# Performance work log

Hardware: AMD Instinct MI355X
Metric: run time of the kernel (lower is better)

The kernel has to match this reference:

```python
import jax, jax.numpy as jnp
import numpy as np

IN_DIM = 128; OUT_DIM = 128; H = 8; DK = OUT_DIM // H
N_A = 100000; N_B = 100000; E0 = 400000; E1 = 400000
NUM_TYPES = 2; NUM_REL = 2
EPS = 1e-9; LN_EPS = 1e-5


def setup_inputs() -> dict:
    key = jax.random.key(0)
    ks = jax.random.split(key, 16)
    s = 0.02
    xav = float(np.sqrt(6.0 / (DK + DK)))  # xavier_uniform bound for (dk, dk)
    inp = {}
    inp['x_a'] = jax.random.normal(ks[0], (N_A, IN_DIM), jnp.float32)
    inp['x_b'] = jax.random.normal(ks[1], (N_B, IN_DIM), jnp.float32)
    inp['ew0'] = jax.random.uniform(ks[2], (E0,), jnp.float32)
    inp['ew1'] = jax.random.uniform(ks[3], (E1,), jnp.float32)
    inp['src0'] = jax.random.randint(ks[4], (E0,), 0, N_A)
    inp['dst0'] = jax.random.randint(ks[5], (E0,), 0, N_B)
    inp['src1'] = jax.random.randint(ks[6], (E1,), 0, N_B)
    inp['dst1'] = jax.random.randint(ks[7], (E1,), 0, N_A)
    # per-node-type stacked linear params: [type, in, out]
    inp['Wk'] = jax.random.normal(ks[8], (NUM_TYPES, IN_DIM, OUT_DIM), jnp.float32) * s
    inp['bk'] = jnp.zeros((NUM_TYPES, OUT_DIM), jnp.float32)
    inp['Wq'] = jax.random.normal(ks[9], (NUM_TYPES, IN_DIM, OUT_DIM), jnp.float32) * s
    inp['bq'] = jnp.zeros((NUM_TYPES, OUT_DIM), jnp.float32)
    inp['Wv'] = jax.random.normal(ks[10], (NUM_TYPES, IN_DIM, OUT_DIM), jnp.float32) * s
    inp['bv'] = jnp.zeros((NUM_TYPES, OUT_DIM), jnp.float32)
    inp['Wa'] = jax.random.normal(ks[11], (NUM_TYPES, OUT_DIM, OUT_DIM), jnp.float32) * s
    inp['ba'] = jnp.zeros((NUM_TYPES, OUT_DIM), jnp.float32)
    inp['ln_g'] = jnp.ones((NUM_TYPES, OUT_DIM), jnp.float32)
    inp['ln_b'] = jnp.zeros((NUM_TYPES, OUT_DIM), jnp.float32)
    inp['rel_pri'] = jnp.ones((NUM_REL, H), jnp.float32)
    inp['rel_att'] = jax.random.uniform(ks[12], (NUM_REL, H, DK, DK), jnp.float32, -xav, xav)
    inp['rel_msg'] = jax.random.uniform(ks[13], (NUM_REL, H, DK, DK), jnp.float32, -xav, xav)
    inp['skip'] = jnp.ones((NUM_TYPES,), jnp.float32)
    return inp


def _edge_softmax(logits, dst, n_dst):
    # segment softmax over incoming edges of each dst node; logits: (E, H)
    m = jax.ops.segment_max(logits, dst, num_segments=n_dst)
    e = jnp.exp(logits - m[dst])
    s = jax.ops.segment_sum(e, dst, num_segments=n_dst)
    return e / s[dst]


def _relation(x_s, x_d, src, dst, ew, Wk_s, bk_s, Wq_d, bq_d, Wv_s, bv_s,
              ratt, rmsg, rpri, n_dst):
    # per-relation HGT attention -> aggregated dst messages (n_dst, H, DK)
    k = (x_s @ Wk_s + bk_s).reshape(-1, H, DK)
    k = jnp.einsum('nhd,hde->nhe', k, ratt)
    v = (x_s @ Wv_s + bv_s).reshape(-1, H, DK)
    v = jnp.einsum('nhd,hde->nhe', v, rmsg)
    q = (x_d @ Wq_d + bq_d).reshape(-1, H, DK)
    t = jnp.einsum('ehd,ehd->eh', q[dst], k[src])  # edge dot score (E, H)
    # dst-normalized edge weight -> additive log bias
    ew = jnp.clip(ew, 0.0)
    den = jax.ops.segment_sum(ew, dst, num_segments=n_dst)
    ewn = ew / jnp.maximum(den[dst], EPS)
    t = t + jnp.log(ewn + EPS)[:, None]
    t = t * rpri / jnp.sqrt(jnp.float32(DK))
    a = _edge_softmax(t, dst, n_dst)  # (E, H)
    msg = v[src] * a[:, :, None]      # (E, H, DK)
    return jax.ops.segment_sum(msg, dst, num_segments=n_dst)


def _forward(x_a, x_b, ew0, ew1, Wk, bk, Wq, bq, Wv, bv, Wa, ba, ln_g, ln_b,
             rel_pri, rel_att, rel_msg, skip, src0, dst0, src1, dst1):
    # relation 0: a -> b (src type 0, dst type 1); relation 1: b -> a
    t_b = _relation(x_a, x_b, src0, dst0, ew0, Wk[0], bk[0], Wq[1], bq[1],
                    Wv[0], bv[0], rel_att[0], rel_msg[0], rel_pri[0], x_b.shape[0])
    t_a = _relation(x_b, x_a, src1, dst1, ew1, Wk[1], bk[1], Wq[0], bq[0],
                    Wv[1], bv[1], rel_att[1], rel_msg[1], rel_pri[1], x_a.shape[0])
    def combine(t, base, nid):
        alpha = jax.nn.sigmoid(skip[nid])
        trans = t.reshape(-1, OUT_DIM) @ Wa[nid] + ba[nid]  # dropout: eval mode
        out = trans * alpha + base * (1.0 - alpha)
        mu = jnp.mean(out, axis=-1, keepdims=True)
        var = jnp.var(out, axis=-1, keepdims=True)
        return (out - mu) / jnp.sqrt(var + LN_EPS) * ln_g[nid] + ln_b[nid]
    return combine(t_a, x_a, 0), combine(t_b, x_b, 1)


def reference(x_a, x_b, ew0, ew1, src0, dst0, src1, dst1, Wk, bk, Wq, bq, Wv, bv,
              Wa, ba, ln_g, ln_b, rel_pri, rel_att, rel_msg, skip):
    return _forward(x_a, x_b, ew0, ew1, Wk, bk, Wq, bq, Wv, bv, Wa, ba, ln_g, ln_b,
                    rel_pri, rel_att, rel_msg, skip, src0, dst0, src1, dst1)
```

## Files before the change

### kernel.cpp

```cpp
#include <hip/hip_runtime.h>
#include <cstdint>
#include <cstddef>

#define EPSF 1e-9f

typedef __bf16 bf16x8 __attribute__((ext_vector_type(8)));
typedef float fvec4 __attribute__((ext_vector_type(4)));

__device__ __forceinline__ float blo(unsigned int u) { return __uint_as_float(u << 16); }
__device__ __forceinline__ float bhi(unsigned int u) { return __uint_as_float(u & 0xffff0000u); }
__device__ __forceinline__ unsigned short f2bf(float f) {
  unsigned int u = __float_as_uint(f);
  u += 0x7fffu + ((u >> 16) & 1u);
  return (unsigned short)(u >> 16);
}
__device__ __forceinline__ unsigned int pack2bf(float a, float b) {
  return (unsigned int)f2bf(a) | ((unsigned int)f2bf(b) << 16);
}

__global__ __launch_bounds__(256) void fzero(float* __restrict__ p, long n) {
  long i = (long)blockIdx.x * blockDim.x + threadIdx.x;
  long stride = (long)gridDim.x * blockDim.x;
  long n4 = n >> 2;
  float4* p4 = (float4*)p;
  for (long j = i; j < n4; j += stride) p4[j] = make_float4(0.f, 0.f, 0.f, 0.f);
  for (long j = (n4 << 2) + i; j < n; j += stride) p[j] = 0.f;
}

__global__ __launch_bounds__(256) void fuse_w(
    const float* __restrict__ Wk, const float* __restrict__ bk,
    const float* __restrict__ Wv, const float* __restrict__ bv,
    const float* __restrict__ rel_att, const float* __restrict__ rel_msg,
    __bf16* __restrict__ WkvqT, float* __restrict__ bkvq)
{
  int i = blockIdx.x;
  int t = blockIdx.y;
  int c = threadIdx.x;
  int m = c >> 7, cc = c & 127;
  int h = cc >> 4, e = cc & 15;
  const float* R = (m ? rel_msg : rel_att) + t * 2048 + h * 256;
  const float* srcW = (m ? Wv : Wk) + t * 16384;
  const float* srcB = (m ? bv : bk) + t * 128;
  const float* row = (i < 128) ? (srcW + i * 128) : srcB;
  float acc = 0.f;
#pragma unroll
  for (int d = 0; d < 16; ++d) acc = fmaf(row[h * 16 + d], R[d * 16 + e], acc);
  if (i < 128) WkvqT[(size_t)t * 49152 + (size_t)c * 128 + i] = (__bf16)acc;
  else         bkvq[t * 384 + c] = acc;
}

__global__ __launch_bounds__(128) void cvt_wT(
    const float* __restrict__ Wq, const float* __restrict__ bq,
    const float* __restrict__ Wa,
    __bf16* __restrict__ WkvqT, __bf16* __restrict__ WaT,
    float* __restrict__ bkvq)
{
  int k = blockIdx.x, t = blockIdx.y, c = threadIdx.x;
  if (blockIdx.z == 0) {
    WkvqT[(size_t)t * 49152 + (size_t)(256 + c) * 128 + k] = (__bf16)Wq[t * 16384 + k * 128 + c];
    if (k == 0) bkvq[t * 384 + 256 + c] = bq[t * 128 + c];
  } else {
    WaT[(size_t)t * 16384 + (size_t)c * 128 + k] = (__bf16)Wa[t * 16384 + k * 128 + c];
  }
}

__global__ __launch_bounds__(256) void gemm_kvq(
    const float* __restrict__ A, int M,
    const __bf16* __restrict__ WT, const float* __restrict__ bias,
    __bf16* __restrict__ KV, __bf16* __restrict__ Q)
{
  __shared__ __bf16 As[64 * 128];
  const int tid = threadIdx.x;
  const int rowb = blockIdx.x * 64;

#pragma unroll
  for (int i = 0; i < 4; ++i) {
    int f = tid + i * 256;
    int r = f >> 4;
    int ch = f & 15;
    int gr = rowb + r; gr = gr < M ? gr : M - 1;
    const float4* ap = (const float4*)(A + (size_t)gr * 128 + ch * 8);
    float4 a0 = ap[0], a1 = ap[1];
    bf16x8 v;
    v[0] = (__bf16)a0.x; v[1] = (__bf16)a0.y; v[2] = (__bf16)a0.z; v[3] = (__bf16)a0.w;
    v[4] = (__bf16)a1.x; v[5] = (__bf16)a1.y; v[6] = (__bf16)a1.z; v[7] = (__bf16)a1.w;
    int sw = (ch * 16) ^ ((r & 7) << 4);
    *(bf16x8*)((char*)As + r * 256 + sw) = v;
  }
  __syncthreads();

  const int l = tid & 63, wid = tid >> 6;
  const int l15 = l & 15, l4 = l >> 4;
  const int wm = wid & 1, wn = wid >> 1;

  bf16x8 af[2][4];
#pragma unroll
  for (int m = 0; m < 2; ++m)
#pragma unroll
    for (int ks = 0; ks < 4; ++ks) {
      int r = wm * 32 + m * 16 + l15;
      int off = (ks * 64 + l4 * 16) ^ ((r & 7) << 4);
      af[m][ks] = *(const bf16x8*)((const char*)As + r * 256 + off);
    }

#pragma unroll
  for (int t = 0; t < 3; ++t) {
    const int colb = t * 128 + wn * 64;
    fvec4 z = {0.f, 0.f, 0.f, 0.f};
    fvec4 acc[2][4];
#pragma unroll
    for (int m = 0; m < 2; ++m)
#pragma unroll
      for (int n = 0; n < 4; ++n) acc[m][n] = z;

    bf16x8 bfr[4][4];
#pragma unroll
    for (int n = 0; n < 4; ++n)
#pragma unroll
      for (int ks = 0; ks < 4; ++ks)
        bfr[n][ks] = *(const bf16x8*)(WT + (size_t)(colb + n * 16 + l15) * 128 + ks * 32 + l4 * 8);

#pragma unroll
    for (int ks = 0; ks < 4; ++ks)
#pragma unroll
      for (int m = 0; m < 2; ++m)
#pragma unroll
        for (int n = 0; n < 4; ++n)
          acc[m][n] = __builtin_amdgcn_mfma_f32_16x16x32_bf16(af[m][ks], bfr[n][ks], acc[m][n], 0, 0, 0);

    __bf16* Cp = (t < 2) ? KV : Q;
    const int ldc = (t < 2) ? 256 : 128;
    const int cbase = (t < 2) ? colb : wn * 64;
#pragma unroll
    for (int m = 0; m < 2; ++m)
#pragma unroll
      for (int n = 0; n < 4; ++n) {
        int col = cbase + n * 16 + l15;
        float bcol = bias[colb + n * 16 + l15];
#pragma unroll
        for (int reg = 0; reg < 4; ++reg) {
          int r = rowb + wm * 32 + m * 16 + l4 * 4 + reg;
          if (r < M) Cp[(size_t)r * ldc + col] = (__bf16)(acc[m][n][reg] + bcol);
        }
      }
  }
}

__global__ __launch_bounds__(256) void csr_count2(
    const int* __restrict__ dst0, int E0, const int* __restrict__ dst1, int E1,
    int* __restrict__ deg, int NB)
{
  int e = blockIdx.x * 256 + threadIdx.x;
  if (e < E0) atomicAdd(&deg[dst0[e]], 1);
  else if (e < E0 + E1) atomicAdd(&deg[NB + dst1[e - E0]], 1);
}

__global__ __launch_bounds__(256) void csr_partial(
    const int* __restrict__ deg, int N, int* __restrict__ partial)
{
  int base = blockIdx.x * 1024 + threadIdx.x * 4;
  int s = 0;
#pragma unroll
  for (int i = 0; i < 4; ++i) if (base + i < N) s += deg[base + i];
#pragma unroll
  for (int m = 1; m < 64; m <<= 1) s += __shfl_xor(s, m, 64);
  __shared__ int wsum[4];
  if ((threadIdx.x & 63) == 0) wsum[threadIdx.x >> 6] = s;
  __syncthreads();
  if (threadIdx.x == 0) partial[blockIdx.x] = wsum[0] + wsum[1] + wsum[2] + wsum[3];
}

__global__ void csr_scan_partials(const int* __restrict__ partial,
                                  int* __restrict__ pscan, int NP)
{
  if (blockIdx.x == 0 && threadIdx.x == 0) {
    int s = 0;
    for (int i = 0; i < NP; ++i) { pscan[i] = s; s += partial[i]; }
  }
}

__global__ __launch_bounds__(256) void csr_scan_chunk(
    const int* __restrict__ deg, const int* __restrict__ pscan,
    int* __restrict__ row_start, int* __restrict__ cursor, int N)
{
  __shared__ int ls[256];
  int base = blockIdx.x * 1024 + threadIdx.x * 4;
  int v0 = 0, v1 = 0, v2 = 0, v3 = 0;
  if (base + 0 < N) v0 = deg[base + 0];
  if (base + 1 < N) v1 = deg[base + 1];
  if (base + 2 < N) v2 = deg[base + 2];
  if (base + 3 < N) v3 = deg[base + 3];
  int s = v0 + v1 + v2 + v3;
  ls[threadIdx.x] = s;
  __syncthreads();
  for (int off = 1; off < 256; off <<= 1) {
    int t = (threadIdx.x >= off) ? ls[threadIdx.x - off] : 0;
    __syncthreads();
    ls[threadIdx.x] += t;
    __syncthreads();
  }
  int excl = pscan[blockIdx.x] + ls[threadIdx.x] - s;
  int p0 = excl, p1 = excl + v0, p2 = excl + v0 + v1, p3 = excl + v0 + v1 + v2;
  if (base + 0 < N) { row_start[base + 0] = p0; cursor[base + 0] = p0; }
  if (base + 1 < N) { row_start[base + 1] = p1; cursor[base + 1] = p1; }
  if (base + 2 < N) { row_start[base + 2] = p2; cursor[base + 2] = p2; }
  if (base + 3 < N) { row_start[base + 3] = p3; cursor[base + 3] = p3; }
}

__global__ __launch_bounds__(256) void csr_scatter2(
    const int* __restrict__ dst0, const int* __restrict__ src0, const float* __restrict__ ew0, int E0,
    const int* __restrict__ dst1, const int* __restrict__ src1, const float* __restrict__ ew1, int E1,
    int* __restrict__ cursor, int* __restrict__ sidx, float* __restrict__ ewc, int NB)
{
  int e = blockIdx.x * 256 + threadIdx.x;
  if (e < E0) {
    int p = atomicAdd(&cursor[dst0[e]], 1);
    sidx[p] = src0[e];
    ewc[p] = fmaxf(ew0[e], 0.f);
  } else if (e < E0 + E1) {
    int e1 = e - E0;
    int p = atomicAdd(&cursor[NB + dst1[e1]], 1);
    sidx[p] = src1[e1];
    ewc[p] = fmaxf(ew1[e1], 0.f);
  }
}

__device__ __forceinline__ void proc_edge(
    float qlo, float qhi, unsigned int ku, unsigned int vu, float w,
    float inv_den, float pr, float& s, float2& acc)
{
  float t = qlo * blo(ku) + qhi * bhi(ku);
  t += __shfl_xor(t, 1, 64);
  t += __shfl_xor(t, 2, 64);
  t += __shfl_xor(t, 4, 64);
  float x = __expf((t + __logf(w * inv_den + EPSF)) * pr);
  s += x;
  acc.x = fmaf(x, blo(vu), acc.x);
  acc.y = fmaf(x, bhi(vu), acc.y);
}

__global__ __launch_bounds__(256) void hgt_dst(
    const __bf16* __restrict__ kvsb, const __bf16* __restrict__ qb,
    const int* __restrict__ row_start, const int* __restrict__ deg,
    const int* __restrict__ sidx, const float* __restrict__ ewc,
    const float* __restrict__ pri8,
    __bf16* __restrict__ agg, int N)
{
  const unsigned short* kvs = (const unsigned short*)kvsb;
  int n = (blockIdx.x * 256 + threadIdx.x) >> 6;
  int lane = threadIdx.x & 63;
  if (n >= N) return;
  int c0 = lane * 2;
  unsigned int* out = (unsigned int*)(agg + (size_t)n * 128 + c0);
  int d = deg[n];
  if (d == 0) { out[0] = 0u; return; }
  int base = row_start[n];

  float ds = 0.f;
  for (int j = lane; j < d; j += 64) ds += ewc[base + j];
#pragma unroll
  for (int m = 1; m < 64; m <<= 1) ds += __shfl_xor(ds, m, 64);
  float inv_den = 1.f / fmaxf(ds, EPSF);

  int h = lane >> 3;
  float pr = pri8[h] * 0.25f;
  unsigned int qu = *(const unsigned int*)((const unsigned short*)qb + (size_t)n * 128 + c0);
  float qlo = blo(qu), qhi = bhi(qu);

  float s = 0.f;
  float2 acc = make_float2(0.f, 0.f);
  int j = 0;
  for (; j + 4 <= d; j += 4) {
    int b = base + j;
    int si0 = sidx[b], si1 = sidx[b + 1], si2 = sidx[b + 2], si3 = sidx[b + 3];
    float w0 = ewc[b], w1 = ewc[b + 1], w2 = ewc[b + 2], w3 = ewc[b + 3];
    const unsigned short* p0 = kvs + (size_t)si0 * 256 + c0;
    const unsigned short* p1 = kvs + (size_t)si1 * 256 + c0;
    const unsigned short* p2 = kvs + (size_t)si2 * 256 + c0;
    const unsigned short* p3 = kvs + (size_t)si3 * 256 + c0;
    unsigned int k0 = *(const unsigned int*)p0, v0 = *(const unsigned int*)(p0 + 128);
    unsigned int k1 = *(const unsigned int*)p1, v1 = *(const unsigned int*)(p1 + 128);
    unsigned int k2 = *(const unsigned int*)p2, v2 = *(const unsigned int*)(p2 + 128);
    unsigned int k3 = *(const unsigned int*)p3, v3 = *(const unsigned int*)(p3 + 128);
    proc_edge(qlo, qhi, k0, v0, w0, inv_den, pr, s, acc);
    proc_edge(qlo, qhi, k1, v1, w1, inv_den, pr, s, acc);
    proc_edge(qlo, qhi, k2, v2, w2, inv_den, pr, s, acc);
    proc_edge(qlo, qhi, k3, v3, w3, inv_den, pr, s, acc);
  }
  for (; j < d; ++j) {
    int b = base + j;
    const unsigned short* p = kvs + (size_t)sidx[b] * 256 + c0;
    proc_edge(qlo, qhi, *(const unsigned int*)p, *(const unsigned int*)(p + 128),
              ewc[b], inv_den, pr, s, acc);
  }
  float is = 1.f / s;
  out[0] = pack2bf(acc.x * is, acc.y * is);
}

__global__ __launch_bounds__(256) void wa_ln(
    const __bf16* __restrict__ Ag, const __bf16* __restrict__ WT,
    const float* __restrict__ bias, const float* __restrict__ xbase,
    const float* __restrict__ g, const float* __restrict__ bb,
    const float* __restrict__ skip, float* __restrict__ out, int M)
{
  int tid = threadIdx.x, l = tid & 63, wid = tid >> 6;
  int l15 = l & 15, l4 = l >> 4;
  int rowb = blockIdx.x * 64 + wid * 16;

  fvec4 z = {0.f, 0.f, 0.f, 0.f};
  fvec4 acc[8];
#pragma unroll
  for (int n = 0; n < 8; ++n) acc[n] = z;

#pragma unroll
  for (int ks = 0; ks < 4; ++ks) {
    int kb = ks * 32 + l4 * 8;
    int r = rowb + l15;
    r = r < M ? r : M - 1;
    bf16x8 af = *(const bf16x8*)(Ag + (size_t)r * 128 + kb);
#pragma unroll
    for (int n = 0; n < 8; ++n) {
      bf16x8 bfr = *(const bf16x8*)(WT + (size_t)(n * 16 + l15) * 128 + kb);
      acc[n] = __builtin_amdgcn_mfma_f32_16x16x32_bf16(af, bfr, acc[n], 0, 0, 0);
    }
  }

  float alpha = 1.f / (1.f + __expf(-skip[0]));
  float onema = 1.f - alpha;
  float o[8][4];
  float psum[4] = {0.f, 0.f, 0.f, 0.f};
  float psq[4] = {0.f, 0.f, 0.f, 0.f};
#pragma unroll
  for (int n = 0; n < 8; ++n) {
    int col = n * 16 + l15;
    float bcol = bias[col];
#pragma unroll
    for (int reg = 0; reg < 4; ++reg) {
      int r = rowb + l4 * 4 + reg;
      float xv = (r < M) ? xbase[(size_t)r * 128 + col] : 0.f;
      float val = (acc[n][reg] + bcol) * alpha + xv * onema;
      o[n][reg] = val;
      psum[reg] += val;
      psq[reg] = fmaf(val, val, psq[reg]);
    }
  }
#pragma unroll
  for (int reg = 0; reg < 4; ++reg) {
#pragma unroll
    for (int m = 1; m < 16; m <<= 1) {
      psum[reg] += __shfl_xor(psum[reg], m, 64);
      psq[reg] += __shfl_xor(psq[reg], m, 64);
    }
  }
  float mu[4], is[4];
#pragma unroll
  for (int reg = 0; reg < 4; ++reg) {
    mu[reg] = psum[reg] * (1.f / 128.f);
    float var = psq[reg] * (1.f / 128.f) - mu[reg] * mu[reg];
    is[reg] = 1.f / sqrtf(var + 1e-5f);
  }
#pragma unroll
  for (int n = 0; n < 8; ++n) {
    int col = n * 16 + l15;
    float gc = g[col], bc = bb[col];
#pragma unroll
    for (int reg = 0; reg < 4; ++reg) {
      int r = rowb + l4 * 4 + reg;
      if (r < M) out[(size_t)r * 128 + col] = (o[n][reg] - mu[reg]) * is[reg] * gc + bc;
    }
  }
}

extern "C" void kernel_launch(void* const* d_in, const int* in_sizes, int n_in,
                              void* d_out, int out_size, void* d_ws, size_t ws_size,
                              hipStream_t stream)
{
  const float* x_a = (const float*)d_in[0];
  const float* x_b = (const float*)d_in[1];
  const float* ew0 = (const float*)d_in[2];
  const float* ew1 = (const float*)d_in[3];
  const int* src0 = (const int*)d_in[4];
  const int* dst0 = (const int*)d_in[5];
  const int* src1 = (const int*)d_in[6];
  const int* dst1 = (const int*)d_in[7];
  const float* Wk = (const float*)d_in[8];
  const float* bk = (const float*)d_in[9];
  const float* Wq = (const float*)d_in[10];
  const float* bq = (const float*)d_in[11];
  const float* Wv = (const float*)d_in[12];
  const float* bv = (const float*)d_in[13];
  const float* Wa = (const float*)d_in[14];
  const float* ba = (const float*)d_in[15];
  const float* ln_g = (const float*)d_in[16];
  const float* ln_b = (const float*)d_in[17];
  const float* rel_pri = (const float*)d_in[18];
  const float* rel_att = (const float*)d_in[19];
  const float* rel_msg = (const float*)d_in[20];
  const float* skip = (const float*)d_in[21];

  int NA = in_sizes[0] / 128, NB = in_sizes[1] / 128;
  int E0 = in_sizes[2], E1 = in_sizes[3];
  int NMAX = NA > NB ? NA : NB;
  int NM = (NMAX + 255) & ~255;
  int N2 = NA + NB;
  int N2M = (N2 + 255) & ~255;
  int E2 = E0 + E1;
  int E2M = (E2 + 255) & ~255;

  char* wsbase = (char*)d_ws;
  size_t off = 0;
  auto alloc = [&](size_t bytes) { char* p = wsbase + off; off += (bytes + 255) & ~(size_t)255; return p; };
  __bf16* kvb_a = (__bf16*)alloc((size_t)NM * 256 * 2);
  __bf16* kvb_b = (__bf16*)alloc((size_t)NM * 256 * 2);
  __bf16* qd_a  = (__bf16*)alloc((size_t)NM * 128 * 2);
  __bf16* qd_b  = (__bf16*)alloc((size_t)NM * 128 * 2);
  __bf16* agg_a = (__bf16*)alloc((size_t)NM * 128 * 2);
  __bf16* agg_b = (__bf16*)alloc((size_t)NM * 128 * 2);
  __bf16* WkvqT = (__bf16*)alloc(2 * 384 * 128 * 2);
  __bf16* WaT   = (__bf16*)alloc(2 * 128 * 128 * 2);
  float* bkvq   = (float*)alloc(2 * 384 * 4);
  int* deg      = (int*)alloc((size_t)N2M * 4);
  int* row_st   = (int*)alloc((size_t)N2M * 4);
  int* cur      = (int*)alloc((size_t)N2M * 4);
  int* partial  = (int*)alloc(1024 * 4);
  int* pscan    = (int*)alloc(1024 * 4);
  int* sidx     = (int*)alloc((size_t)E2M * 4);
  float* ewc    = (float*)alloc((size_t)E2M * 4);

  float* outf = (float*)d_out;
  dim3 b256(256);
  auto cdiv = [](int a, int b) { return (unsigned)((a + b - 1) / b); };

  fuse_w<<<dim3(129, 2), b256, 0, stream>>>(Wk, bk, Wv, bv, rel_att, rel_msg, WkvqT, bkvq);
  cvt_wT<<<dim3(128, 2, 2), 128, 0, stream>>>(Wq, bq, Wa, WkvqT, WaT, bkvq);

  int NP = (N2 + 1023) / 1024;
  fzero<<<64, b256, 0, stream>>>((float*)deg, N2);
  csr_count2<<<cdiv(E2, 256), b256, 0, stream>>>(dst0, E0, dst1, E1, deg, NB);
  csr_partial<<<NP, b256, 0, stream>>>(deg, N2, partial);
  csr_scan_partials<<<1, 64, 0, stream>>>(partial, pscan, NP);
  csr_scan_chunk<<<NP, b256, 0, stream>>>(deg, pscan, row_st, cur, N2);
  csr_scatter2<<<cdiv(E2, 256), b256, 0, stream>>>(dst0, src0, ew0, E0,
                                                   dst1, src1, ew1, E1,
                                                   cur, sidx, ewc, NB);

  gemm_kvq<<<cdiv(NA, 64), b256, 0, stream>>>(x_a, NA, WkvqT, bkvq, kvb_a, qd_a);
  gemm_kvq<<<cdiv(NB, 64), b256, 0, stream>>>(x_b, NB, WkvqT + 49152, bkvq + 384, kvb_b, qd_b);

  hgt_dst<<<cdiv(NB, 4), b256, 0, stream>>>(kvb_a, qd_b, row_st, deg, sidx, ewc,
                                            rel_pri, agg_b, NB);
  hgt_dst<<<cdiv(NA, 4), b256, 0, stream>>>(kvb_b, qd_a, row_st + NB, deg + NB, sidx, ewc,
                                            rel_pri + 8, agg_a, NA);

  wa_ln<<<cdiv(NA, 64), b256, 0, stream>>>(agg_a, WaT, ba, x_a, ln_g, ln_b, skip, outf, NA);
  wa_ln<<<cdiv(NB, 64), b256, 0, stream>>>(agg_b, WaT + 16384, ba + 128, x_b,
                                           ln_g + 128, ln_b + 128, skip + 1,
                                           outf + (size_t)NA * 128, NB);
}
```

Before: 627.3 us.

## Merge per-type launches and transpose MFMA operands for vectorized stores

Merges the paired launches of the KVQ GEMM, the destination aggregation and the Wa+LayerNorm kernels into one launch each, picking the node type from the block index. It also swaps the MFMA operand order so each lane holds four consecutive columns of one row. Epilogues can then use packed bf16 and float4 stores, with vector bias, gamma, beta and residual loads. LayerNorm reductions shrink to two cross-lane shuffles. The aim is to cut launch gaps and tail effects and to coalesce output writes, at the cost of some extra select logic per block.

```diff
diff --git a/kernel.cpp b/kernel.cpp
--- a/kernel.cpp
+++ b/kernel.cpp
@@ -65,19 +65,27 @@
 }
 
 __global__ __launch_bounds__(256) void gemm_kvq(
-    const float* __restrict__ A, int M,
-    const __bf16* __restrict__ WT, const float* __restrict__ bias,
-    __bf16* __restrict__ KV, __bf16* __restrict__ Q)
+    const float* __restrict__ Aa, int Ma, const float* __restrict__ Ab, int Mb, int nblk_a,
+    const __bf16* __restrict__ WTall, const float* __restrict__ ball,
+    __bf16* __restrict__ KVa, __bf16* __restrict__ Qa,
+    __bf16* __restrict__ KVb, __bf16* __restrict__ Qb)
 {
   __shared__ __bf16 As[64 * 128];
   const int tid = threadIdx.x;
-  const int rowb = blockIdx.x * 64;
+  const bool isA = blockIdx.x < (unsigned)nblk_a;
+  const int blk = isA ? blockIdx.x : blockIdx.x - nblk_a;
+  const float* A = isA ? Aa : Ab;
+  const int M = isA ? Ma : Mb;
+  const __bf16* WT = WTall + (isA ? 0 : 49152);
+  const float* bs = ball + (isA ? 0 : 384);
+  __bf16* KV = isA ? KVa : KVb;
+  __bf16* Q  = isA ? Qa : Qb;
+  const int rowb = blk * 64;
 
 #pragma unroll
   for (int i = 0; i < 4; ++i) {
     int f = tid + i * 256;
-    int r = f >> 4;
-    int ch = f & 15;
+    int r = f >> 4, ch = f & 15;
     int gr = rowb + r; gr = gr < M ? gr : M - 1;
     const float4* ap = (const float4*)(A + (size_t)gr * 128 + ch * 8);
     float4 a0 = ap[0], a1 = ap[1];
@@ -126,23 +134,23 @@
       for (int m = 0; m < 2; ++m)
 #pragma unroll
         for (int n = 0; n < 4; ++n)
-          acc[m][n] = __builtin_amdgcn_mfma_f32_16x16x32_bf16(af[m][ks], bfr[n][ks], acc[m][n], 0, 0, 0);
-
-    __bf16* Cp = (t < 2) ? KV : Q;
-    const int ldc = (t < 2) ? 256 : 128;
-    const int cbase = (t < 2) ? colb : wn * 64;
-#pragma unroll
-    for (int m = 0; m < 2; ++m)
+          acc[m][n] = __builtin_amdgcn_mfma_f32_16x16x32_bf16(bfr[n][ks], af[m][ks], acc[m][n], 0, 0, 0);
+
+#pragma unroll
+    for (int m = 0; m < 2; ++m) {
+      int r = rowb + wm * 32 + m * 16 + l15;
+      if (r >= M) continue;
 #pragma unroll
       for (int n = 0; n < 4; ++n) {
-        int col = cbase + n * 16 + l15;
-        float bcol = bias[colb + n * 16 + l15];
-#pragma unroll
-        for (int reg = 0; reg < 4; ++reg) {
-          int r = rowb + wm * 32 + m * 16 + l4 * 4 + reg;
-          if (r < M) Cp[(size_t)r * ldc + col] = (__bf16)(acc[m][n][reg] + bcol);
-        }
+        int cb = colb + n * 16 + l4 * 4;
+        fvec4 b4 = *(const fvec4*)(bs + cb);
+        uint2 w;
+        w.x = pack2bf(acc[m][n][0] + b4[0], acc[m][n][1] + b4[1]);
+        w.y = pack2bf(acc[m][n][2] + b4[2], acc[m][n][3] + b4[3]);
+        if (t < 2) *(uint2*)(KV + (size_t)r * 256 + cb) = w;
+        else       *(uint2*)(Q + (size_t)r * 128 + (cb - 256)) = w;
       }
+    }
   }
 }
 
@@ -240,18 +248,23 @@
 }
 
 __global__ __launch_bounds__(256) void hgt_dst(
-    const __bf16* __restrict__ kvsb, const __bf16* __restrict__ qb,
+    const __bf16* __restrict__ kv0, const __bf16* __restrict__ q0,
+    const __bf16* __restrict__ kv1, const __bf16* __restrict__ q1,
     const int* __restrict__ row_start, const int* __restrict__ deg,
     const int* __restrict__ sidx, const float* __restrict__ ewc,
-    const float* __restrict__ pri8,
-    __bf16* __restrict__ agg, int N)
-{
-  const unsigned short* kvs = (const unsigned short*)kvsb;
+    const float* __restrict__ pri16,
+    __bf16* __restrict__ agg0, __bf16* __restrict__ agg1, int NB, int N2)
+{
   int n = (blockIdx.x * 256 + threadIdx.x) >> 6;
   int lane = threadIdx.x & 63;
-  if (n >= N) return;
+  if (n >= N2) return;
+  bool g0 = n < NB;
+  int nl = g0 ? n : n - NB;
+  const unsigned short* kvs = (const unsigned short*)(g0 ? kv0 : kv1);
+  const unsigned short* qrow = (const unsigned short*)(g0 ? q0 : q1) + (size_t)nl * 128;
+  const float* pri8 = pri16 + (g0 ? 0 : 8);
   int c0 = lane * 2;
-  unsigned int* out = (unsigned int*)(agg + (size_t)n * 128 + c0);
+  unsigned int* out = (unsigned int*)((g0 ? agg0 : agg1) + (size_t)nl * 128 + c0);
   int d = deg[n];
   if (d == 0) { out[0] = 0u; return; }
   int base = row_start[n];
@@ -264,7 +277,7 @@
 
   int h = lane >> 3;
   float pr = pri8[h] * 0.25f;
-  unsigned int qu = *(const unsigned int*)((const unsigned short*)qb + (size_t)n * 128 + c0);
+  unsigned int qu = *(const unsigned int*)(qrow + c0);
   float qlo = blo(qu), qhi = bhi(qu);
 
   float s = 0.f;
@@ -298,75 +311,80 @@
 }
 
 __global__ __launch_bounds__(256) void wa_ln(
-    const __bf16* __restrict__ Ag, const __bf16* __restrict__ WT,
-    const float* __restrict__ bias, const float* __restrict__ xbase,
-    const float* __restrict__ g, const float* __restrict__ bb,
-    const float* __restrict__ skip, float* __restrict__ out, int M)
-{
-  int tid = threadIdx.x, l = tid & 63, wid = tid >> 6;
-  int l15 = l & 15, l4 = l >> 4;
-  int rowb = blockIdx.x * 64 + wid * 16;
+    const __bf16* __restrict__ Ag_a, const __bf16* __restrict__ Ag_b,
+    const __bf16* __restrict__ WaT, const float* __restrict__ ba,
+    const float* __restrict__ x_a, const float* __restrict__ x_b,
+    const float* __restrict__ lng, const float* __restrict__ lnb,
+    const float* __restrict__ skip, float* __restrict__ out,
+    int NA, int NB, int nblk_a)
+{
+  const int tid = threadIdx.x, l = tid & 63, wid = tid >> 6;
+  const int l15 = l & 15, l4 = l >> 4;
+  const bool isA = blockIdx.x < (unsigned)nblk_a;
+  const int blk = isA ? blockIdx.x : blockIdx.x - nblk_a;
+  const int M = isA ? NA : NB;
+  const __bf16* Ag = isA ? Ag_a : Ag_b;
+  const __bf16* WT = WaT + (isA ? 0 : 16384);
+  const float* bias = ba + (isA ? 0 : 128);
+  const float* xb = isA ? x_a : x_b;
+  const float* g = lng + (isA ? 0 : 128);
+  const float* bb = lnb + (isA ? 0 : 128);
+  float* o = out + (isA ? (size_t)0 : (size_t)NA * 128);
+  const int rowb = blk * 64 + wid * 16;
+  const int r = rowb + l15;
+  const int rc = r < M ? r : M - 1;
+
+  bf16x8 af[4];
+#pragma unroll
+  for (int ks = 0; ks < 4; ++ks)
+    af[ks] = *(const bf16x8*)(Ag + (size_t)rc * 128 + ks * 32 + l4 * 8);
 
   fvec4 z = {0.f, 0.f, 0.f, 0.f};
   fvec4 acc[8];
 #pragma unroll
   for (int n = 0; n < 8; ++n) acc[n] = z;
-
-#pragma unroll
-  for (int ks = 0; ks < 4; ++ks) {
-    int kb = ks * 32 + l4 * 8;
-    int r = rowb + l15;
-    r = r < M ? r : M - 1;
-    bf16x8 af = *(const bf16x8*)(Ag + (size_t)r * 128 + kb);
+#pragma unroll
+  for (int ks = 0; ks < 4; ++ks)
 #pragma unroll
     for (int n = 0; n < 8; ++n) {
-      bf16x8 bfr = *(const bf16x8*)(WT + (size_t)(n * 16 + l15) * 128 + kb);
-      acc[n] = __builtin_amdgcn_mfma_f32_16x16x32_bf16(af, bfr, acc[n], 0, 0, 0);
+      bf16x8 wf = *(const bf16x8*)(WT + (size_t)(n * 16 + l15) * 128 + ks * 32 + l4 * 8);
+      acc[n] = __builtin_amdgcn_mfma_f32_16x16x32_bf16(wf, af[ks], acc[n], 0, 0, 0);
     }
-  }
-
-  float alpha = 1.f / (1.f + __expf(-skip[0]));
+
+  float alpha = 1.f / (1.f + __expf(-skip[isA ? 0 : 1]));
   float onema = 1.f - alpha;
-  float o[8][4];
-  float psum[4] = {0.f, 0.f, 0.f, 0.f};
-  float psq[4] = {0.f, 0.f, 0.f, 0.f};
+  float vals[8][4];
+  float psum = 0.f, psq = 0.f;
 #pragma unroll
   for (int n = 0; n < 8; ++n) {
-    int col = n * 16 + l15;
-    float bcol = bias[col];
+    int cb = n * 16 + l4 * 4;
+    fvec4 b4 = *(const fvec4*)(bias + cb);
+    fvec4 xv = *(const fvec4*)(xb + (size_t)rc * 128 + cb);
 #pragma unroll
     for (int reg = 0; reg < 4; ++reg) {
-      int r = rowb + l4 * 4 + reg;
-      float xv = (r < M) ? xbase[(size_t)r * 128 + col] : 0.f;
-      float val = (acc[n][reg] + bcol) * alpha + xv * onema;
-      o[n][reg] = val;
-      psum[reg] += val;
-      psq[reg] = fmaf(val, val, psq[reg]);
+      float v = (acc[n][reg] + b4[reg]) * alpha + xv[reg] * onema;
+      vals[n][reg] = v;
+      psum += v;
+      psq = fmaf(v, v, psq);
     }
   }
-#pragma unroll
-  for (int reg = 0; reg < 4; ++reg) {
-#pragma unroll
-    for (int m = 1; m < 16; m <<= 1) {
-      psum[reg] += __shfl_xor(psum[reg], m, 64);
-      psq[reg] += __shfl_xor(psq[reg], m, 64);
-    }
-  }
-  float mu[4], is[4];
-#pragma unroll
-  for (int reg = 0; reg < 4; ++reg) {
-    mu[reg] = psum[reg] * (1.f / 128.f);
-    float var = psq[reg] * (1.f / 128.f) - mu[reg] * mu[reg];
-    is[reg] = 1.f / sqrtf(var + 1e-5f);
-  }
-#pragma unroll
-  for (int n = 0; n < 8; ++n) {
-    int col = n * 16 + l15;
-    float gc = g[col], bc = bb[col];
-#pragma unroll
-    for (int reg = 0; reg < 4; ++reg) {
-      int r = rowb + l4 * 4 + reg;
-      if (r < M) out[(size_t)r * 128 + col] = (o[n][reg] - mu[reg]) * is[reg] * gc + bc;
+  psum += __shfl_xor(psum, 16, 64); psq += __shfl_xor(psq, 16, 64);
+  psum += __shfl_xor(psum, 32, 64); psq += __shfl_xor(psq, 32, 64);
+  float mu = psum * (1.f / 128.f);
+  float var = psq * (1.f / 128.f) - mu * mu;
+  float is = 1.f / sqrtf(var + 1e-5f);
+
+  if (r < M) {
+#pragma unroll
+    for (int n = 0; n < 8; ++n) {
+      int cb = n * 16 + l4 * 4;
+      fvec4 g4 = *(const fvec4*)(g + cb);
+      fvec4 bb4 = *(const fvec4*)(bb + cb);
+      fvec4 ov;
+#pragma unroll
+      for (int reg = 0; reg < 4; ++reg)
+        ov[reg] = (vals[n][reg] - mu) * is * g4[reg] + bb4[reg];
+      *(fvec4*)(o + (size_t)r * 128 + cb) = ov;
     }
   }
 }
@@ -444,16 +462,14 @@
                                                    dst1, src1, ew1, E1,
                                                    cur, sidx, ewc, NB);
 
-  gemm_kvq<<<cdiv(NA, 64), b256, 0, stream>>>(x_a, NA, WkvqT, bkvq, kvb_a, qd_a);
-  gemm_kvq<<<cdiv(NB, 64), b256, 0, stream>>>(x_b, NB, WkvqT + 49152, bkvq + 384, kvb_b, qd_b);
-
-  hgt_dst<<<cdiv(NB, 4), b256, 0, stream>>>(kvb_a, qd_b, row_st, deg, sidx, ewc,
-                                            rel_pri, agg_b, NB);
-  hgt_dst<<<cdiv(NA, 4), b256, 0, stream>>>(kvb_b, qd_a, row_st + NB, deg + NB, sidx, ewc,
-                                            rel_pri + 8, agg_a, NA);
-
-  wa_ln<<<cdiv(NA, 64), b256, 0, stream>>>(agg_a, WaT, ba, x_a, ln_g, ln_b, skip, outf, NA);
-  wa_ln<<<cdiv(NB, 64), b256, 0, stream>>>(agg_b, WaT + 16384, ba + 128, x_b,
-                                           ln_g + 128, ln_b + 128, skip + 1,
-                                           outf + (size_t)NA * 128, NB);
-}
+  int nba = cdiv(NA, 64), nbb = cdiv(NB, 64);
+  gemm_kvq<<<nba + nbb, b256, 0, stream>>>(x_a, NA, x_b, NB, nba, WkvqT, bkvq,
+                                           kvb_a, qd_a, kvb_b, qd_b);
+
+  hgt_dst<<<cdiv(N2, 4), b256, 0, stream>>>(kvb_a, qd_b, kvb_b, qd_a,
+                                            row_st, deg, sidx, ewc, rel_pri,
+                                            agg_b, agg_a, NB, N2);
+
+  wa_ln<<<nba + nbb, b256, 0, stream>>>(agg_a, agg_b, WaT, ba, x_a, x_b,
+                                        ln_g, ln_b, skip, outf, NA, NB, nba);
+}
```

After: 582.8 us. 7.1% less time.
